# Kernel optimization log

Measured on AMD Instinct MI355X. Metric: run time of the kernel, lower is better.

Reference implementation:

```python
import jax, jax.numpy as jnp
import numpy as np

N_NODES = 50000
EMBED_DIM = 512
N_EDGES = 150000


def _edge_scores(node_embeddings, edges):
    # edges: [2, E] int; dot product of endpoint embeddings -> [E]
    src = node_embeddings[edges[0]]  # [E, D]
    dst = node_embeddings[edges[1]]  # [E, D]
    return jnp.sum(src * dst, axis=1)


def setup_inputs() -> dict:
    key = jax.random.key(0)
    k1, k2, k3 = jax.random.split(key, 3)
    node_embeddings = jax.random.normal(k1, (N_NODES, EMBED_DIM), dtype=jnp.float32)
    edge_index = jax.random.randint(k2, (2, N_EDGES), 0, N_NODES, dtype=jnp.int64)
    # negative edges: uniform random node pairs (matches the original sampler's
    # fallback distribution; precomputed so the reference is deterministic/jittable)
    neg_edges = jax.random.randint(k3, (2, N_EDGES), 0, N_NODES, dtype=jnp.int64)
    return {
        "node_embeddings": node_embeddings,
        "edge_index": edge_index,
        "neg_edges": neg_edges,
        "num_nodes": N_NODES,
    }


def reference(node_embeddings, edge_index, neg_edges, num_nodes):
    pos_scores = _edge_scores(node_embeddings, edge_index)  # [E]
    neg_scores = _edge_scores(node_embeddings, neg_edges)   # [E]
    all_scores = jnp.concatenate([pos_scores, neg_scores])
    all_labels = jnp.concatenate([
        jnp.ones_like(pos_scores),
        jnp.zeros_like(neg_scores),
    ])
    # BCE with logits: log(1 + exp(s)) - s*y, numerically stable via logaddexp
    per_elem = jnp.logaddexp(jnp.float32(0.0), all_scores) - all_scores * all_labels
    return jnp.mean(per_elem)
```

## Files before the change

kernel.cpp:

```cpp
#include <hip/hip_runtime.h>
#include <math.h>

#define N_EDGES   150000
#define TOTAL     300000
#define EMBED_DIM 512
#define N_NODES   50000
#define TABLE_ELEMS (N_NODES * EMBED_DIM)
#define TABLE_BYTES_F8 ((size_t)TABLE_ELEMS)
#define BLOCK_THREADS 256
#define CONV_BLOCKS 2048

#define GROUPS16   (TOTAL / 16)
#define POS_G16    (N_EDGES / 16)

#define NCHUNK       8
#define CHUNK_BYTES  64
#define SLICE_BYTES  ((size_t)N_NODES * CHUNK_BYTES)
#define PARTIAL_BYTES ((size_t)NCHUNK * TOTAL * 4)
#define WS_ACC_OFF   (TABLE_BYTES_F8 + PARTIAL_BYTES)
#define WS_CLAIM_OFF (WS_ACC_OFF + 64)
#define WS_NEEDED    (WS_CLAIM_OFF + 8 * 64)

#define SCORE_BLOCKS 2048
#define SPAN_G   16
#define BATCH    8
#define RED_BLOCKS ((TOTAL + BLOCK_THREADS - 1) / BLOCK_THREADS)

typedef float floatx4 __attribute__((ext_vector_type(4)));
typedef unsigned long long ull;
typedef ull ull2 __attribute__((ext_vector_type(2)));

__global__ __launch_bounds__(BLOCK_THREADS) void convert_fp8_chunked(
    const float4* __restrict__ in,
    int*          __restrict__ out,
    float*        __restrict__ acc,
    unsigned int* __restrict__ cnt,
    int*          __restrict__ claim)
{
    if (blockIdx.x == 0 && threadIdx.x < 128) {
        if (threadIdx.x == 0) { *acc = 0.0f; *cnt = 0u; }
        claim[threadIdx.x] = 0;
    }
    const int stride = gridDim.x * blockDim.x;
    for (int o = blockIdx.x * blockDim.x + threadIdx.x;
         o < TABLE_ELEMS / 4; o += stride) {
        const int chunk = o / (N_NODES * 16);
        const int rem   = o - chunk * (N_NODES * 16);
        const int node  = rem >> 4;
        const int w4    = rem & 15;
        float4 v = in[node * 128 + chunk * 16 + w4];
        int r = 0;
        r = __builtin_amdgcn_cvt_pk_fp8_f32(v.x, v.y, r, false);
        r = __builtin_amdgcn_cvt_pk_fp8_f32(v.z, v.w, r, true);
        out[o] = r;
    }
}

__global__ __launch_bounds__(BLOCK_THREADS, 4) void edge_score_chunked(
    const unsigned char* __restrict__ emb8,
    const int*           __restrict__ pos_edges,
    const int*           __restrict__ neg_edges,
    float*               __restrict__ partial,
    int*                 __restrict__ claim)
{
    unsigned int xcc;
    asm volatile("s_getreg_b32 %0, hwreg(HW_REG_XCC_ID)" : "=s"(xcc));
    const int chunk = (int)(xcc & 7u);

    const int lane = threadIdx.x & 63;
    const int i    = lane & 15;
    const int quad = lane >> 4;
    const bool is_diag = ((i >> 2) == quad);
    const int  dreg    = i & 3;

    const unsigned char* __restrict__ slice = emb8 + (size_t)chunk * SLICE_BYTES;
    float* __restrict__ pout = partial + (size_t)chunk * TOTAL;

    for (;;) {
        int base0 = 0;
        if (lane == 0) base0 = atomicAdd(claim + chunk * 16, SPAN_G);
        const int base = __builtin_amdgcn_readfirstlane(base0);
        if (base >= GROUPS16) break;

        int sA[BATCH], tA[BATCH];
        #pragma unroll
        for (int j = 0; j < BATCH; j++) {
            const int g  = base + j;
            const int gc = (g < GROUPS16) ? g : (GROUPS16 - 1);
            const bool ip = (gc < POS_G16);
            const int* __restrict__ ed = ip ? pos_edges : neg_edges;
            const int e0 = 16 * gc - (ip ? 0 : N_EDGES);
            sA[j] = __builtin_nontemporal_load(ed + e0 + i);
            tA[j] = __builtin_nontemporal_load(ed + N_EDGES + e0 + i);
        }
        ull2 aA[BATCH], bA[BATCH];
        #pragma unroll
        for (int j = 0; j < BATCH; j++) {
            aA[j] = *(const ull2*)(slice + (size_t)(unsigned)sA[j] * CHUNK_BYTES + quad * 16);
            bA[j] = *(const ull2*)(slice + (size_t)(unsigned)tA[j] * CHUNK_BYTES + quad * 16);
        }
        int sB[BATCH], tB[BATCH];
        #pragma unroll
        for (int j = 0; j < BATCH; j++) {
            const int g  = base + BATCH + j;
            const int gc = (g < GROUPS16) ? g : (GROUPS16 - 1);
            const bool ip = (gc < POS_G16);
            const int* __restrict__ ed = ip ? pos_edges : neg_edges;
            const int e0 = 16 * gc - (ip ? 0 : N_EDGES);
            sB[j] = __builtin_nontemporal_load(ed + e0 + i);
            tB[j] = __builtin_nontemporal_load(ed + N_EDGES + e0 + i);
        }
#if __has_builtin(__builtin_amdgcn_sched_barrier)
        __builtin_amdgcn_sched_barrier(0);
#endif
        #pragma unroll
        for (int j = 0; j < BATCH; j++) {
            floatx4 C = {0, 0, 0, 0};
            C = __builtin_amdgcn_mfma_f32_16x16x32_fp8_fp8((long)aA[j][0], (long)bA[j][0], C, 0, 0, 0);
            C = __builtin_amdgcn_mfma_f32_16x16x32_fp8_fp8((long)aA[j][1], (long)bA[j][1], C, 0, 0, 0);
            const float s = (dreg == 0) ? C[0] : (dreg == 1) ? C[1] : (dreg == 2) ? C[2] : C[3];
            const int g = base + j;
            if (is_diag && g < GROUPS16)
                __builtin_nontemporal_store(s, pout + 16 * g + i);
        }
        ull2 aB[BATCH], bB[BATCH];
        #pragma unroll
        for (int j = 0; j < BATCH; j++) {
            aB[j] = *(const ull2*)(slice + (size_t)(unsigned)sB[j] * CHUNK_BYTES + quad * 16);
            bB[j] = *(const ull2*)(slice + (size_t)(unsigned)tB[j] * CHUNK_BYTES + quad * 16);
        }
#if __has_builtin(__builtin_amdgcn_sched_barrier)
        __builtin_amdgcn_sched_barrier(0);
#endif
        #pragma unroll
        for (int j = 0; j < BATCH; j++) {
            floatx4 C = {0, 0, 0, 0};
            C = __builtin_amdgcn_mfma_f32_16x16x32_fp8_fp8((long)aB[j][0], (long)bB[j][0], C, 0, 0, 0);
            C = __builtin_amdgcn_mfma_f32_16x16x32_fp8_fp8((long)aB[j][1], (long)bB[j][1], C, 0, 0, 0);
            const float s = (dreg == 0) ? C[0] : (dreg == 1) ? C[1] : (dreg == 2) ? C[2] : C[3];
            const int g = base + BATCH + j;
            if (is_diag && g < GROUPS16)
                __builtin_nontemporal_store(s, pout + 16 * g + i);
        }
    }
}

__global__ __launch_bounds__(BLOCK_THREADS) void reduce_bce_finalize(
    const float*  __restrict__ partial,
    float*        __restrict__ acc,
    unsigned int* __restrict__ cnt,
    float*        __restrict__ out)
{
    const int e = blockIdx.x * BLOCK_THREADS + threadIdx.x;
    float term = 0.0f;
    if (e < TOTAL) {
        float s = 0.0f;
        #pragma unroll
        for (int c = 0; c < NCHUNK; c++)
            s += partial[(size_t)c * TOTAL + e];
        const float sp = fmaxf(s, 0.0f) + log1pf(expf(-fabsf(s)));
        term = sp - (e < N_EDGES ? s : 0.0f);
    }
    #pragma unroll
    for (int off = 32; off > 0; off >>= 1)
        term += __shfl_down(term, off, 64);
    __shared__ float ls[4];
    if ((threadIdx.x & 63) == 0) ls[threadIdx.x >> 6] = term;
    __syncthreads();
    if (threadIdx.x == 0) {
        atomicAdd(acc, ls[0] + ls[1] + ls[2] + ls[3]);
        __threadfence();
        const unsigned prev = atomicAdd(cnt, 1u);
        if (prev == (unsigned)(gridDim.x - 1)) {
            __threadfence();
            const float tot = atomicAdd(acc, 0.0f);
            out[0] = tot * (1.0f / (float)TOTAL);
        }
    }
}

__global__ __launch_bounds__(BLOCK_THREADS) void convert_fp8(
    const float4* __restrict__ in,
    int*          __restrict__ out,
    float*        __restrict__ acc)
{
    if (blockIdx.x == 0 && threadIdx.x == 0) *acc = 0.0f;
    const int stride = gridDim.x * blockDim.x;
    for (int i = blockIdx.x * blockDim.x + threadIdx.x;
         i < TABLE_ELEMS / 4; i += stride) {
        float4 v = in[i];
        int r = 0;
        r = __builtin_amdgcn_cvt_pk_fp8_f32(v.x, v.y, r, false);
        r = __builtin_amdgcn_cvt_pk_fp8_f32(v.z, v.w, r, true);
        out[i] = r;
    }
}

#define EDGE_BLOCKS ((GROUPS16 + 3) / 4)
__global__ __launch_bounds__(BLOCK_THREADS, 4) void edge_loss_fp8(
    const unsigned char* __restrict__ emb8,
    const int*           __restrict__ pos_edges,
    const int*           __restrict__ neg_edges,
    float*               __restrict__ acc)
{
    const int wave = threadIdx.x >> 6;
    const int lane = threadIdx.x & 63;
    const int g    = blockIdx.x * 4 + wave;
    const int i    = lane & 15;
    const int quad = lane >> 4;
    const bool is_diag = ((i >> 2) == quad);
    const int  dreg    = i & 3;
    float contrib = 0.0f;
    if (g < GROUPS16) {
        const bool is_pos = (g < POS_G16);
        const int* __restrict__ edges = is_pos ? pos_edges : neg_edges;
        const int  e0 = 16 * g - (is_pos ? 0 : N_EDGES);
        const int sidx = edges[e0 + i];
        const int tidx = edges[N_EDGES + e0 + i];
        const ull2* rA = (const ull2*)(emb8 + (size_t)sidx * EMBED_DIM + quad * 16);
        const ull2* rB = (const ull2*)(emb8 + (size_t)tidx * EMBED_DIM + quad * 16);
        ull2 a[8], b[8];
        #pragma unroll
        for (int c = 0; c < 8; c++) { a[c] = rA[c * 4]; b[c] = rB[c * 4]; }
#if __has_builtin(__builtin_amdgcn_sched_barrier)
        __builtin_amdgcn_sched_barrier(0);
#endif
        floatx4 C0 = {0,0,0,0}, C1 = {0,0,0,0}, C2 = {0,0,0,0}, C3 = {0,0,0,0};
        #pragma unroll
        for (int c = 0; c < 2; c++) {
            #pragma unroll
            for (int h = 0; h < 2; h++) {
                C0 = __builtin_amdgcn_mfma_f32_16x16x32_fp8_fp8((long)a[c][h],     (long)b[c][h],     C0, 0, 0, 0);
                C1 = __builtin_amdgcn_mfma_f32_16x16x32_fp8_fp8((long)a[2 + c][h], (long)b[2 + c][h], C1, 0, 0, 0);
                C2 = __builtin_amdgcn_mfma_f32_16x16x32_fp8_fp8((long)a[4 + c][h], (long)b[4 + c][h], C2, 0, 0, 0);
                C3 = __builtin_amdgcn_mfma_f32_16x16x32_fp8_fp8((long)a[6 + c][h], (long)b[6 + c][h], C3, 0, 0, 0);
            }
        }
        floatx4 C = (C0 + C1) + (C2 + C3);
        float s = (dreg == 0) ? C[0] : (dreg == 1) ? C[1] : (dreg == 2) ? C[2] : C[3];
        float sp = fmaxf(s, 0.0f) + log1pf(expf(-fabsf(s)));
        contrib = is_diag ? (sp - (is_pos ? s : 0.0f)) : 0.0f;
    }
    #pragma unroll
    for (int off = 32; off > 0; off >>= 1)
        contrib += __shfl_down(contrib, off, 64);
    __shared__ float ls[4];
    if (lane == 0) ls[wave] = contrib;
    __syncthreads();
    if (threadIdx.x == 0)
        atomicAdd(acc, ls[0] + ls[1] + ls[2] + ls[3]);
}

#define N_PAIRS   (TOTAL / 2)
#define POS_PAIRS (N_EDGES / 2)
#define FB_WAVES  (CONV_BLOCKS * 4)
__global__ __launch_bounds__(BLOCK_THREADS, 8) void edge_loss_f32(
    const float* __restrict__ emb,
    const int*   __restrict__ pos_edges,
    const int*   __restrict__ neg_edges,
    float*       __restrict__ acc)
{
    const int wave  = threadIdx.x >> 6;
    const int lane  = threadIdx.x & 63;
    const int gwave = blockIdx.x * 4 + wave;
    float lsum = 0.0f;
    for (int g = gwave; g < N_PAIRS; g += FB_WAVES) {
        const bool is_pos = (g < POS_PAIRS);
        const int* __restrict__ edges = is_pos ? pos_edges : neg_edges;
        const int  e0 = 2 * g - (is_pos ? 0 : N_EDGES);
        const int s0 = edges[e0],     t0 = edges[N_EDGES + e0];
        const int s1 = edges[e0 + 1], t1 = edges[N_EDGES + e0 + 1];
        const float4* rS0 = (const float4*)(emb + (size_t)s0 * EMBED_DIM) + lane;
        const float4* rT0 = (const float4*)(emb + (size_t)t0 * EMBED_DIM) + lane;
        const float4* rS1 = (const float4*)(emb + (size_t)s1 * EMBED_DIM) + lane;
        const float4* rT1 = (const float4*)(emb + (size_t)t1 * EMBED_DIM) + lane;
        float4 a0 = rS0[0], a1 = rS0[64];
        float4 b0 = rT0[0], b1 = rT0[64];
        float4 c0 = rS1[0], c1 = rS1[64];
        float4 d0 = rT1[0], d1 = rT1[64];
        float p0 = fmaf(a0.x, b0.x, fmaf(a0.y, b0.y, fmaf(a0.z, b0.z, a0.w * b0.w)));
        float p1 = fmaf(a1.x, b1.x, fmaf(a1.y, b1.y, fmaf(a1.z, b1.z, a1.w * b1.w)));
        float q0 = fmaf(c0.x, d0.x, fmaf(c0.y, d0.y, fmaf(c0.z, d0.z, c0.w * d0.w)));
        float q1 = fmaf(c1.x, d1.x, fmaf(c1.y, d1.y, fmaf(c1.z, d1.z, c1.w * d1.w)));
        float p = p0 + p1, q = q0 + q1;
        #pragma unroll
        for (int off = 32; off > 0; off >>= 1) {
            p += __shfl_down(p, off, 64);
            q += __shfl_down(q, off, 64);
        }
        const float sp_p = fmaxf(p, 0.0f) + log1pf(expf(-fabsf(p)));
        const float sp_q = fmaxf(q, 0.0f) + log1pf(expf(-fabsf(q)));
        lsum += (lane == 0) ? (sp_p + sp_q - (is_pos ? (p + q) : 0.0f)) : 0.0f;
    }
    __shared__ float ls[4];
    if (lane == 0) ls[wave] = lsum;
    __syncthreads();
    if (threadIdx.x == 0)
        atomicAdd(acc, ls[0] + ls[1] + ls[2] + ls[3]);
}

__global__ void finalize_kernel(const float* __restrict__ acc, float* __restrict__ out)
{
    if (threadIdx.x == 0)
        out[0] = acc[0] * (1.0f / (float)TOTAL);
}

extern "C" void kernel_launch(void* const* d_in, const int* in_sizes, int n_in,
                              void* d_out, int out_size, void* d_ws, size_t ws_size,
                              hipStream_t stream) {
    const float* emb = (const float*)d_in[0];
    const int*   pos = (const int*)d_in[1];
    const int*   neg = (const int*)d_in[2];
    float* out = (float*)d_out;

    if (ws_size >= WS_NEEDED) {
        unsigned char* emb8    = (unsigned char*)d_ws;
        float*         partial = (float*)((char*)d_ws + TABLE_BYTES_F8);
        float*         acc     = (float*)((char*)d_ws + WS_ACC_OFF);
        unsigned int*  cnt     = (unsigned int*)((char*)d_ws + WS_ACC_OFF + 4);
        int*           claim   = (int*)((char*)d_ws + WS_CLAIM_OFF);
        convert_fp8_chunked<<<CONV_BLOCKS, BLOCK_THREADS, 0, stream>>>(
            (const float4*)emb, (int*)d_ws, acc, cnt, claim);
        edge_score_chunked<<<SCORE_BLOCKS, BLOCK_THREADS, 0, stream>>>(
            emb8, pos, neg, partial, claim);
        reduce_bce_finalize<<<RED_BLOCKS, BLOCK_THREADS, 0, stream>>>(
            partial, acc, cnt, out);
    } else if (ws_size >= TABLE_BYTES_F8 + 64) {
        unsigned char* emb8 = (unsigned char*)d_ws;
        float*         acc  = (float*)((char*)d_ws + TABLE_BYTES_F8);
        convert_fp8<<<CONV_BLOCKS, BLOCK_THREADS, 0, stream>>>(
            (const float4*)emb, (int*)d_ws, acc);
        edge_loss_fp8<<<EDGE_BLOCKS, BLOCK_THREADS, 0, stream>>>(emb8, pos, neg, acc);
        finalize_kernel<<<1, 64, 0, stream>>>(acc, out);
    } else {
        float* acc = (float*)d_ws;
        (void)hipMemsetAsync(acc, 0, sizeof(float), stream);
        edge_loss_f32<<<CONV_BLOCKS, BLOCK_THREADS, 0, stream>>>(emb, pos, neg, acc);
        finalize_kernel<<<1, 64, 0, stream>>>(acc, out);
    }
}
```

Baseline: 257.1 us.

## Replace XCC-based atomic work claiming with static blockIdx chunk mapping and vectorized index loads

The edge-score kernel no longer reads the XCC ID and claims work through per-chunk atomic counters. It now derives the chunk from blockIdx and strides waves statically over the groups. Edge indices are loaded as wide int2 vectors and redistributed with shuffles instead of per-lane scalar loads. The conversion kernel processes all 8 chunks per node unit in one loop. Together these remove the atomic contention and cut the number of index load instructions. The cost is that locality now relies on the hardware assigning block IDs round-robin across XCCs, and there is no dynamic load balancing.

Measured after the change: 234.4 us. 8.8% less time.

```diff
diff --git a/kernel.cpp b/kernel.cpp
--- a/kernel.cpp
+++ b/kernel.cpp
@@ -15,13 +15,14 @@
 
 #define NCHUNK       8
 #define CHUNK_BYTES  64
+#define NODE_UNITS   (N_NODES * 16)
 #define SLICE_BYTES  ((size_t)N_NODES * CHUNK_BYTES)
 #define PARTIAL_BYTES ((size_t)NCHUNK * TOTAL * 4)
 #define WS_ACC_OFF   (TABLE_BYTES_F8 + PARTIAL_BYTES)
-#define WS_CLAIM_OFF (WS_ACC_OFF + 64)
-#define WS_NEEDED    (WS_CLAIM_OFF + 8 * 64)
+#define WS_NEEDED    (WS_ACC_OFF + 64)
 
 #define SCORE_BLOCKS 2048
+#define WAVES_PER_CHUNK 1024
 #define SPAN_G   16
 #define BATCH    8
 #define RED_BLOCKS ((TOTAL + BLOCK_THREADS - 1) / BLOCK_THREADS)
@@ -29,30 +30,65 @@
 typedef float floatx4 __attribute__((ext_vector_type(4)));
 typedef unsigned long long ull;
 typedef ull ull2 __attribute__((ext_vector_type(2)));
+typedef int  intx2 __attribute__((ext_vector_type(2)));
 
 __global__ __launch_bounds__(BLOCK_THREADS) void convert_fp8_chunked(
     const float4* __restrict__ in,
     int*          __restrict__ out,
     float*        __restrict__ acc,
-    unsigned int* __restrict__ cnt,
-    int*          __restrict__ claim)
-{
-    if (blockIdx.x == 0 && threadIdx.x < 128) {
-        if (threadIdx.x == 0) { *acc = 0.0f; *cnt = 0u; }
-        claim[threadIdx.x] = 0;
-    }
+    unsigned int* __restrict__ cnt)
+{
+    if (blockIdx.x == 0 && threadIdx.x == 0) { *acc = 0.0f; *cnt = 0u; }
     const int stride = gridDim.x * blockDim.x;
-    for (int o = blockIdx.x * blockDim.x + threadIdx.x;
-         o < TABLE_ELEMS / 4; o += stride) {
-        const int chunk = o / (N_NODES * 16);
-        const int rem   = o - chunk * (N_NODES * 16);
-        const int node  = rem >> 4;
-        const int w4    = rem & 15;
-        float4 v = in[node * 128 + chunk * 16 + w4];
-        int r = 0;
-        r = __builtin_amdgcn_cvt_pk_fp8_f32(v.x, v.y, r, false);
-        r = __builtin_amdgcn_cvt_pk_fp8_f32(v.z, v.w, r, true);
-        out[o] = r;
+    for (int u = blockIdx.x * blockDim.x + threadIdx.x;
+         u < NODE_UNITS; u += stride) {
+        const int node = u >> 4;
+        const int w4   = u & 15;
+        const float4* __restrict__ src = in + node * 128 + w4;
+        #pragma unroll
+        for (int c = 0; c < NCHUNK; c++) {
+            float4 v = src[c * 16];
+            int r = 0;
+            r = __builtin_amdgcn_cvt_pk_fp8_f32(v.x, v.y, r, false);
+            r = __builtin_amdgcn_cvt_pk_fp8_f32(v.z, v.w, r, true);
+            out[c * NODE_UNITS + u] = r;
+        }
+    }
+}
+
+__device__ __forceinline__ void load_idx_batch(
+    int gb, int i, int half, int sl8,
+    const int* __restrict__ pos_edges, const int* __restrict__ neg_edges,
+    int* __restrict__ s, int* __restrict__ t)
+{
+    const bool widepos = (gb + BATCH <= POS_G16);
+    const bool wideneg = (gb >= POS_G16) && (16 * gb + 128 <= 2 * N_EDGES);
+    if (widepos || wideneg) {
+        const int* __restrict__ ed = widepos ? pos_edges : neg_edges;
+        const int e0 = 16 * gb - (widepos ? 0 : N_EDGES);
+        const int lane = (threadIdx.x & 63);
+        const intx2 sv = __builtin_nontemporal_load((const intx2*)(ed + e0) + lane);
+        const intx2 tv = __builtin_nontemporal_load((const intx2*)(ed + N_EDGES + e0) + lane);
+        #pragma unroll
+        for (int j = 0; j < BATCH; j++) {
+            const int sx = __shfl(sv[0], 8 * j + sl8, 64);
+            const int sy = __shfl(sv[1], 8 * j + sl8, 64);
+            s[j] = half ? sy : sx;
+            const int tx = __shfl(tv[0], 8 * j + sl8, 64);
+            const int ty = __shfl(tv[1], 8 * j + sl8, 64);
+            t[j] = half ? ty : tx;
+        }
+    } else {
+        #pragma unroll
+        for (int j = 0; j < BATCH; j++) {
+            int g = gb + j;
+            if (g > GROUPS16 - 1) g = GROUPS16 - 1;
+            const bool ip = (g < POS_G16);
+            const int* __restrict__ ed = ip ? pos_edges : neg_edges;
+            const int e0 = 16 * g - (ip ? 0 : N_EDGES);
+            s[j] = __builtin_nontemporal_load(ed + e0 + i);
+            t[j] = __builtin_nontemporal_load(ed + N_EDGES + e0 + i);
+        }
     }
 }
 
@@ -60,55 +96,32 @@
     const unsigned char* __restrict__ emb8,
     const int*           __restrict__ pos_edges,
     const int*           __restrict__ neg_edges,
-    float*               __restrict__ partial,
-    int*                 __restrict__ claim)
-{
-    unsigned int xcc;
-    asm volatile("s_getreg_b32 %0, hwreg(HW_REG_XCC_ID)" : "=s"(xcc));
-    const int chunk = (int)(xcc & 7u);
-
-    const int lane = threadIdx.x & 63;
-    const int i    = lane & 15;
-    const int quad = lane >> 4;
+    float*               __restrict__ partial)
+{
+    const int chunk = blockIdx.x & 7;
+    const int wid   = (blockIdx.x >> 3) * 4 + (threadIdx.x >> 6);
+    const int lane  = threadIdx.x & 63;
+    const int i     = lane & 15;
+    const int quad  = lane >> 4;
     const bool is_diag = ((i >> 2) == quad);
-    const int  dreg    = i & 3;
+    const int  dreg = i & 3;
+    const int  half = i & 1;
+    const int  sl8  = i >> 1;
 
     const unsigned char* __restrict__ slice = emb8 + (size_t)chunk * SLICE_BYTES;
     float* __restrict__ pout = partial + (size_t)chunk * TOTAL;
 
-    for (;;) {
-        int base0 = 0;
-        if (lane == 0) base0 = atomicAdd(claim + chunk * 16, SPAN_G);
-        const int base = __builtin_amdgcn_readfirstlane(base0);
-        if (base >= GROUPS16) break;
-
-        int sA[BATCH], tA[BATCH];
-        #pragma unroll
-        for (int j = 0; j < BATCH; j++) {
-            const int g  = base + j;
-            const int gc = (g < GROUPS16) ? g : (GROUPS16 - 1);
-            const bool ip = (gc < POS_G16);
-            const int* __restrict__ ed = ip ? pos_edges : neg_edges;
-            const int e0 = 16 * gc - (ip ? 0 : N_EDGES);
-            sA[j] = __builtin_nontemporal_load(ed + e0 + i);
-            tA[j] = __builtin_nontemporal_load(ed + N_EDGES + e0 + i);
-        }
+    for (int base = wid * SPAN_G; base < GROUPS16;
+         base += WAVES_PER_CHUNK * SPAN_G) {
+        int sA[BATCH], tA[BATCH], sB[BATCH], tB[BATCH];
+        load_idx_batch(base,         i, half, sl8, pos_edges, neg_edges, sA, tA);
+        load_idx_batch(base + BATCH, i, half, sl8, pos_edges, neg_edges, sB, tB);
+
         ull2 aA[BATCH], bA[BATCH];
         #pragma unroll
         for (int j = 0; j < BATCH; j++) {
             aA[j] = *(const ull2*)(slice + (size_t)(unsigned)sA[j] * CHUNK_BYTES + quad * 16);
             bA[j] = *(const ull2*)(slice + (size_t)(unsigned)tA[j] * CHUNK_BYTES + quad * 16);
-        }
-        int sB[BATCH], tB[BATCH];
-        #pragma unroll
-        for (int j = 0; j < BATCH; j++) {
-            const int g  = base + BATCH + j;
-            const int gc = (g < GROUPS16) ? g : (GROUPS16 - 1);
-            const bool ip = (gc < POS_G16);
-            const int* __restrict__ ed = ip ? pos_edges : neg_edges;
-            const int e0 = 16 * gc - (ip ? 0 : N_EDGES);
-            sB[j] = __builtin_nontemporal_load(ed + e0 + i);
-            tB[j] = __builtin_nontemporal_load(ed + N_EDGES + e0 + i);
         }
 #if __has_builtin(__builtin_amdgcn_sched_barrier)
         __builtin_amdgcn_sched_barrier(0);
@@ -318,11 +331,10 @@
         float*         partial = (float*)((char*)d_ws + TABLE_BYTES_F8);
         float*         acc     = (float*)((char*)d_ws + WS_ACC_OFF);
         unsigned int*  cnt     = (unsigned int*)((char*)d_ws + WS_ACC_OFF + 4);
-        int*           claim   = (int*)((char*)d_ws + WS_CLAIM_OFF);
         convert_fp8_chunked<<<CONV_BLOCKS, BLOCK_THREADS, 0, stream>>>(
-            (const float4*)emb, (int*)d_ws, acc, cnt, claim);
+            (const float4*)emb, (int*)d_ws, acc, cnt);
         edge_score_chunked<<<SCORE_BLOCKS, BLOCK_THREADS, 0, stream>>>(
-            emb8, pos, neg, partial, claim);
+            emb8, pos, neg, partial);
         reduce_bce_finalize<<<RED_BLOCKS, BLOCK_THREADS, 0, stream>>>(
             partial, acc, cnt, out);
     } else if (ws_size >= TABLE_BYTES_F8 + 64) {
```
